# Kernel tuning notes

Measured on AMD Instinct MI355X. Metric: run time of the kernel, lower is better.

## Reference

```python
import jax, jax.numpy as jnp
import numpy as np
from jax import lax

B, T, D, H = 64, 2048, 128, 256  # batch, seq_len, input_dim, hidden_dim


def setup_inputs() -> dict:
    key = jax.random.key(0)
    ks = jax.random.split(key, 21)
    s = 0.05
    p = lambda k, shape: jax.random.normal(k, shape, dtype=jnp.float32) * s
    inp = {"x": jax.random.normal(ks[0], (B, T, D), dtype=jnp.float32)}
    i = 1
    for n in ["e1", "e2", "d1", "d2"]:  # encode1, encode2, reconstruct1, reconstruct2
        inp[n + "_Wih"] = p(ks[i], (4 * H, D)); i += 1
        inp[n + "_Whh"] = p(ks[i], (4 * H, H)); i += 1
        inp[n + "_bih"] = p(ks[i], (4 * H,)); i += 1
        inp[n + "_bhh"] = p(ks[i], (4 * H,)); i += 1
    inp["l1_W"] = p(ks[17], (D, H)); inp["l1_b"] = p(ks[18], (D,))
    inp["l2_W"] = p(ks[19], (D, H)); inp["l2_b"] = p(ks[20], (D,))
    return inp


def _lstm_cell(h, c, xt, Wih, Whh, bih, bhh):
    # PyTorch gate order: i, f, g, o
    g = xt @ Wih.T + h @ Whh.T + bih + bhh  # [B, 4H]
    i, f, gg, o = jnp.split(g, 4, axis=-1)
    c = jax.nn.sigmoid(f) * c + jax.nn.sigmoid(i) * jnp.tanh(gg)
    h = jax.nn.sigmoid(o) * jnp.tanh(c)
    return h, c


def _encode(x, h0, c0, Wih, Whh, bih, bhh):
    # x: [B, T, D] batch_first -> scan over time
    def step(carry, xt):
        h, c = carry
        h, c = _lstm_cell(h, c, xt, Wih, Whh, bih, bhh)
        return (h, c), None
    (h, c), _ = lax.scan(step, (h0, c0), jnp.swapaxes(x, 0, 1))
    return h, c


def _decode(n, h, c, Wih, Whh, bih, bhh, Wl, bl):
    # first output is linear(hidden) before any cell step (matches original decode)
    inp0 = h @ Wl.T + bl  # [B, D]
    def step(carry, _):
        h, c, inp = carry
        h, c = _lstm_cell(h, c, inp, Wih, Whh, bih, bhh)
        inp = h @ Wl.T + bl
        return (h, c, inp), inp
    _, outs = lax.scan(step, (h, c, inp0), None, length=n - 1)  # [n-1, B, D]
    out = jnp.concatenate([inp0[None], outs], axis=0)  # [n, B, D]
    return jnp.swapaxes(out, 0, 1)  # [B, n, D]


def reference(x,
              e1_Wih, e1_Whh, e1_bih, e1_bhh,
              e2_Wih, e2_Whh, e2_bih, e2_bhh,
              d1_Wih, d1_Whh, d1_bih, d1_bhh,
              d2_Wih, d2_Whh, d2_bih, d2_bhh,
              l1_W, l1_b, l2_W, l2_b):
    Bc, Tc = x.shape[0], x.shape[1]
    T1 = Tc // 2
    h0 = jnp.zeros((Bc, H), dtype=x.dtype)
    c0 = jnp.zeros((Bc, H), dtype=x.dtype)
    x1 = x[:, :T1][:, ::-1]  # first half, time-reversed
    x2 = x[:, T1:]
    h1, c1 = _encode(x1, h0, c0, e1_Wih, e1_Whh, e1_bih, e1_bhh)
    h2, c2 = _encode(x2, h1, c1, e2_Wih, e2_Whh, e2_bih, e2_bhh)
    out1 = _decode(T1, h1, c1, d1_Wih, d1_Whh, d1_bih, d1_bhh, l1_W, l1_b)
    out2 = _decode(Tc - T1, h2, c2, d2_Wih, d2_Whh, d2_bih, d2_bhh, l2_W, l2_b)[:, ::-1]
    return jnp.concatenate([out1, out2], axis=1)  # [B, T, D]
```

## Files before the change

kernel.cpp:

```cpp
#include <hip/hip_runtime.h>
#include <stdint.h>

#define Bv 64
#define Tv 2048
#define T1v 1024
#define Dv 128
#define Hv 256

typedef _Float16 h2_t __attribute__((ext_vector_type(2)));

__device__ inline float d2(uint32_t hp, uint32_t wp, float acc) {
#if __has_builtin(__builtin_amdgcn_fdot2)
  return __builtin_amdgcn_fdot2(__builtin_bit_cast(h2_t, hp),
                                __builtin_bit_cast(h2_t, wp), acc, false);
#else
  float out;
  asm("v_dot2_f32_f16 %0, %1, %2, %3" : "=v"(out) : "v"(hp), "v"(wp), "v"(acc));
  return out;
#endif
}

__device__ inline uint16_t f2h(float x) {
  _Float16 h = (_Float16)x;
  return __builtin_bit_cast(uint16_t, h);
}
__device__ inline float h2f(uint16_t u) {
  return (float)__builtin_bit_cast(_Float16, u);
}
__device__ inline uint32_t packpair(float a, float b) {
  return (uint32_t)f2h(a) | ((uint32_t)f2h(b) << 16);
}
__device__ inline float unpk(uint32_t u, int hi) {
  return h2f((uint16_t)(hi ? (u >> 16) : (u & 0xffff)));
}
__device__ inline float sigm(float x) { return 1.f / (1.f + __expf(-x)); }
__device__ inline float tanh_(float x) { return 2.f / (1.f + __expf(-2.f * x)) - 1.f; }

__device__ inline float qsum4(float v) {
  int t = __builtin_amdgcn_update_dpp(0, __float_as_int(v), 0xB1, 0xF, 0xF, true);
  v += __int_as_float(t);
  t = __builtin_amdgcn_update_dpp(0, __float_as_int(v), 0x4E, 0xF, 0xF, true);
  return v + __int_as_float(t);
}

__device__ inline uint4 ld_stream(const uint4* p) {
  const volatile uint32_t* q = (const volatile uint32_t*)p;
  uint4 v;
  v.x = q[0];
  v.y = q[1];
  v.z = q[2];
  v.w = q[3];
  return v;
}


__global__ void k_pack_x(const float* __restrict__ x, uint32_t* __restrict__ xpk) {
  int idx = blockIdx.x * 256 + threadIdx.x;
  const float2* x2 = (const float2*)x;
  float2 v = x2[idx];
  xpk[idx] = packpair(v.x, v.y);
}

__global__ void k_pack_w(const float* __restrict__ src, uint32_t* __restrict__ wAll,
                         uint32_t* __restrict__ wLg, uint32_t* __restrict__ wStr) {
  int idx = blockIdx.x * 256 + threadIdx.x;
  int row = idx >> 7, k2 = idx & 127;
  uint32_t pr = packpair(src[row * 256 + 2 * k2], src[row * 256 + 2 * k2 + 1]);
  wAll[k2 * 1024 + row] = pr;
  if (k2 >= 96) {
    int g = (k2 - 96) >> 2, qq = (k2 - 96) & 3;
    wLg[(g * 1024 + row) * 4 + qq] = pr;
  }
  if (k2 >= 48 && k2 < 96) wStr[row * 48 + (k2 - 48)] = pr;
}

__global__ void k_pack_w2(const float* __restrict__ src, uint32_t* __restrict__ wSt,
                          uint32_t* __restrict__ wLds) {
  int idx = blockIdx.x * 256 + threadIdx.x;
  int r = idx >> 7, k2 = idx & 127;
  uint32_t pr = packpair(src[r * 256 + 2 * k2], src[r * 256 + 2 * k2 + 1]);
  int gate = r >> 8, u = r & 255;
  int u_hi = u >> 7, jb = u & 127;
  int q = k2 >> 5, kk = k2 & 31;
  int tid = jb * 4 + q;
  int ri = u_hi * 4 + gate;
  if (kk < 24) {
    wSt[((ri * 6 + (kk >> 2)) * 512 + tid) * 4 + (kk & 3)] = pr;
  } else {
    wLds[((ri * 2 + ((kk - 24) >> 2)) * 512 + tid) * 4 + ((kk - 24) & 3)] = pr;
  }
}

__global__ void k_bias_pack(const float* __restrict__ b32, uint32_t* __restrict__ bpk) {
  int jb = threadIdx.x;
  uint32_t w[4];
#pragma unroll
  for (int wi = 0; wi < 4; ++wi) {
    int ri0 = 2 * wi, ri1 = 2 * wi + 1;
    int row0 = (ri0 & 3) * 256 + jb + 128 * (ri0 >> 2);
    int row1 = (ri1 & 3) * 256 + jb + 128 * (ri1 >> 2);
    w[wi] = packpair(b32[row0], b32[row1]);
  }
  ((uint4*)bpk)[jb] = make_uint4(w[0], w[1], w[2], w[3]);
}

__global__ void k_pack_wih(const float* __restrict__ Wih, uint32_t* __restrict__ wihp) {
  int idx = blockIdx.x * 256 + threadIdx.x;
  int row = idx >> 6, k2 = idx & 63;
  wihp[row * 64 + k2] = packpair(Wih[row * 128 + 2 * k2], Wih[row * 128 + 2 * k2 + 1]);
}

__global__ void k_bias2(const float* __restrict__ bih, const float* __restrict__ bhh,
                        float* __restrict__ bias) {
  int i = blockIdx.x * 256 + threadIdx.x;
  if (i < 1024) bias[i] = bih[i] + bhh[i];
}

__global__ void k_dec_combine(const float* __restrict__ Whh, const float* __restrict__ Wih,
                              const float* __restrict__ bih, const float* __restrict__ bhh,
                              const float* __restrict__ lW, const float* __restrict__ lb,
                              float* __restrict__ wd, float* __restrict__ bias) {
  int j = blockIdx.x;
  int k = threadIdx.x;
  __shared__ float wr[128];
  if (k < 128) wr[k] = Wih[j * 128 + k];
  __syncthreads();
  float acc = Whh[j * 256 + k];
  for (int d = 0; d < 128; ++d) acc += wr[d] * lW[d * 256 + k];
  wd[j * 256 + k] = acc;
  if (k == 0) {
    float s = bih[j] + bhh[j];
    for (int d = 0; d < 128; ++d) s += wr[d] * lb[d];
    bias[j] = s;
  }
}

__global__ void k_pack_wl(const float* __restrict__ lW, uint32_t* __restrict__ wlp) {
  int idx = blockIdx.x * 256 + threadIdx.x;
  int d = idx >> 7, k2 = idx & 127;
  wlp[d * 128 + k2] = packpair(lW[d * 256 + 2 * k2], lW[d * 256 + 2 * k2 + 1]);
}

template <int LAY>
__global__ __launch_bounds__(256) void k_xp_gemm(const uint32_t* __restrict__ xpk,
                                                 const uint32_t* __restrict__ wihp,
                                                 uint16_t* __restrict__ xp, int xt0, int xdt) {
  const int b = blockIdx.z;
  const int s0 = blockIdx.y * 32;
  const int r = blockIdx.x * 256 + threadIdx.x;
  uint32_t wreg[64];
#pragma unroll
  for (int k = 0; k < 64; ++k) wreg[k] = wihp[r * 64 + k];
  const int gate = r >> 8, u = r & 255;
  const int u_hi = u >> 7, jb = u & 127;
  const int ri = u_hi * 4 + gate;
  for (int sl = 0; sl < 32; ++sl) {
    const int s = s0 + sl;
    const int t = xt0 + s * xdt;
    const uint32_t* __restrict__ xrow = xpk + ((size_t)b * Tv + t) * 64;
    float a0 = 0.f, a1 = 0.f;
#pragma unroll
    for (int k = 0; k < 64; k += 2) {
      a0 = d2(xrow[k], wreg[k], a0);
      a1 = d2(xrow[k + 1], wreg[k + 1], a1);
    }
    uint16_t v = f2h(a0 + a1);
    if (LAY == 0)
      xp[(((size_t)b * T1v + s) * 128 + jb) * 8 + ri] = v;
    else
      xp[((size_t)b * T1v + s) * 1024 + r] = v;
  }
}


struct CfgU {
  const uint4* wSt;
  const uint4* wLds;
  const uint4* bpk;
  const uint4* xps;
  const float* h0;
  const float* c0;
  float* hN;
  float* cN;
  uint16_t* hist;
};

template <int NREGC, int NSTRC, int NLDSC>
__global__ void __launch_bounds__(512)
__attribute__((amdgpu_waves_per_eu(2, 2)))
k_rnnU(CfgU cA, CfgU cB, int nA) {
  __shared__ __align__(16) uint4 wldsM[NLDSC * 8 * 512];
  __shared__ __align__(16) uint16_t hbuf[2][4][72];

  const bool isA = (int)blockIdx.x < nA;
  const CfgU cfg = isA ? cA : cB;
  const int b = isA ? (int)blockIdx.x : ((int)blockIdx.x - nA);
  const int tid = threadIdx.x;
  const int q = tid & 3, jb = tid >> 2;

#pragma unroll
  for (int ri = 0; ri < 8; ++ri)
#pragma unroll
    for (int li = 0; li < NLDSC; ++li)
      wldsM[(ri * NLDSC + li) * 512 + tid] =
          cfg.wLds[(ri * 2 + (2 - NLDSC) + li) * 512 + tid];

  uint4 wr[8][NREGC];
#pragma unroll
  for (int ri = 0; ri < 8; ++ri)
#pragma unroll
    for (int cc = 0; cc < NREGC; ++cc) wr[ri][cc] = cfg.wSt[(ri * 6 + cc) * 512 + tid];

  const uint4 bp = cfg.bpk[jb];
  float c0r = cfg.c0 ? cfg.c0[b * 256 + jb] : 0.f;
  float c1r = cfg.c0 ? cfg.c0[b * 256 + jb + 128] : 0.f;

  uint16_t* histp = cfg.hist ? cfg.hist + (size_t)b * 1024 * 256 : nullptr;
  if (q == 0) {
    float h00 = cfg.h0 ? cfg.h0[b * 256 + jb] : 0.f;
    float h01 = cfg.h0 ? cfg.h0[b * 256 + jb + 128] : 0.f;
    uint16_t u0 = f2h(h00), u1 = f2h(h01);
    hbuf[0][jb >> 6][jb & 63] = u0;
    hbuf[0][2 + (jb >> 6)][jb & 63] = u1;
    if (histp) {
      histp[jb] = u0;
      histp[jb + 128] = u1;
    }
  }
  const uint4* xps4 = cfg.xps ? cfg.xps + (size_t)b * 1024 * 128 + jb : nullptr;

  __syncthreads();

  int cur = 0;
  for (int s = 0; s < 1024; ++s) {
    uint4 xq = make_uint4(0, 0, 0, 0);
    if (xps4) xq = xps4[(size_t)s * 128];
    const uint4* Hq = (const uint4*)&hbuf[cur][q][0];

    float acc[8];
#pragma unroll
    for (int ri = 0; ri < 8; ++ri) acc[ri] = 0.f;

#pragma unroll
    for (int cc = 0; cc < NREGC; ++cc) {
      const uint4 hv = Hq[cc];
#pragma unroll
      for (int ri = 0; ri < 8; ++ri) {
        acc[ri] = d2(hv.x, wr[ri][cc].x, acc[ri]);
        acc[ri] = d2(hv.y, wr[ri][cc].y, acc[ri]);
        acc[ri] = d2(hv.z, wr[ri][cc].z, acc[ri]);
        acc[ri] = d2(hv.w, wr[ri][cc].w, acc[ri]);
      }
    }
#pragma unroll
    for (int j = 0; j < NSTRC; ++j) {
      const int cc = NREGC + j;
      const uint4 hv = Hq[cc];
#pragma unroll
      for (int ri = 0; ri < 8; ++ri) {
        const uint4 wv = (cc < 6) ? ld_stream(cfg.wSt + (ri * 6 + cc) * 512 + tid)
                                  : ld_stream(cfg.wLds + (ri * 2 + (cc - 6)) * 512 + tid);
        acc[ri] = d2(hv.x, wv.x, acc[ri]);
        acc[ri] = d2(hv.y, wv.y, acc[ri]);
        acc[ri] = d2(hv.z, wv.z, acc[ri]);
        acc[ri] = d2(hv.w, wv.w, acc[ri]);
      }
    }
#pragma unroll
    for (int li = 0; li < NLDSC; ++li) {
      const int cc = 8 - NLDSC + li;
      const uint4 hv = Hq[cc];
#pragma unroll
      for (int ri = 0; ri < 8; ++ri) {
        const uint4 wv = wldsM[(ri * NLDSC + li) * 512 + tid];
        acc[ri] = d2(hv.x, wv.x, acc[ri]);
        acc[ri] = d2(hv.y, wv.y, acc[ri]);
        acc[ri] = d2(hv.z, wv.z, acc[ri]);
        acc[ri] = d2(hv.w, wv.w, acc[ri]);
      }
    }

#pragma unroll
    for (int ri = 0; ri < 8; ++ri) acc[ri] = qsum4(acc[ri]);

    acc[0] += unpk(bp.x, 0) + unpk(xq.x, 0);
    acc[1] += unpk(bp.x, 1) + unpk(xq.x, 1);
    acc[2] += unpk(bp.y, 0) + unpk(xq.y, 0);
    acc[3] += unpk(bp.y, 1) + unpk(xq.y, 1);
    acc[4] += unpk(bp.z, 0) + unpk(xq.z, 0);
    acc[5] += unpk(bp.z, 1) + unpk(xq.z, 1);
    acc[6] += unpk(bp.w, 0) + unpk(xq.w, 0);
    acc[7] += unpk(bp.w, 1) + unpk(xq.w, 1);

    const float cn0 = sigm(acc[1]) * c0r + sigm(acc[0]) * tanh_(acc[2]);
    const float h0v = sigm(acc[3]) * tanh_(cn0);
    c0r = cn0;
    const float cn1 = sigm(acc[5]) * c1r + sigm(acc[4]) * tanh_(acc[6]);
    const float h1v = sigm(acc[7]) * tanh_(cn1);
    c1r = cn1;

    if (q == 0) {
      const uint16_t hu0 = f2h(h0v), hu1 = f2h(h1v);
      hbuf[cur ^ 1][jb >> 6][jb & 63] = hu0;
      hbuf[cur ^ 1][2 + (jb >> 6)][jb & 63] = hu1;
      if (histp && s < 1023) {
        histp[(size_t)(s + 1) * 256 + jb] = hu0;
        histp[(size_t)(s + 1) * 256 + jb + 128] = hu1;
      }
    }
    __syncthreads();
    cur ^= 1;
  }

  if (cfg.hN && q == 0) {
    cfg.hN[b * 256 + jb] = h2f(hbuf[cur][jb >> 6][jb & 63]);
    cfg.hN[b * 256 + jb + 128] = h2f(hbuf[cur][2 + (jb >> 6)][jb & 63]);
    cfg.cN[b * 256 + jb] = c0r;
    cfg.cN[b * 256 + jb + 128] = c1r;
  }
}


struct ChainCfg {
  const uint32_t* wAll;
  const uint4* wLg;
  const uint32_t* wStr;
  const uint32_t* wih;
  const uint32_t* xpk;
  const uint16_t* xps;
  const float* bias;
  const float* h0;
  const float* c0;
  float* hN;
  float* cN;
  uint16_t* hist;
  int xt0, xdt;
};

template <int NRESP, bool WIH>
__global__ void __launch_bounds__(512)
__attribute__((amdgpu_waves_per_eu(2, 2)))
k_rnn5(ChainCfg cA, ChainCfg cB, int nA) {
  __shared__ __align__(16) uint4 wlds4[8 * 1024];
  __shared__ float gsm[1024];
  __shared__ __align__(16) uint16_t h16[256];
  __shared__ __align__(16) uint32_t xsh[64];

  const bool isA = (int)blockIdx.x < nA;
  const ChainCfg cfg = isA ? cA : cB;
  const int b = isA ? (int)blockIdx.x : ((int)blockIdx.x - nA);
  const int tid = threadIdx.x;
  const int r0 = tid, r1 = tid + 512;

#pragma unroll
  for (int i = 0; i < 16; ++i) wlds4[i * 512 + tid] = cfg.wLg[i * 512 + tid];

  uint16_t* histp = cfg.hist ? cfg.hist + (size_t)b * 1024 * 256 : nullptr;

  float creg = 0.f;
  if (tid < 256) {
    float h0v = cfg.h0 ? cfg.h0[b * 256 + tid] : 0.f;
    creg = cfg.c0 ? cfg.c0[b * 256 + tid] : 0.f;
    uint16_t hu = f2h(h0v);
    h16[tid] = hu;
    if (histp) histp[tid] = hu;
  }

  uint32_t w0[NRESP], w1[NRESP];
#pragma unroll
  for (int k = 0; k < NRESP; ++k) w0[k] = cfg.wAll[k * 1024 + r0];
#pragma unroll
  for (int k = 0; k < NRESP; ++k) w1[k] = cfg.wAll[k * 1024 + r1];
  const float bias0 = cfg.bias[r0];
  const float bias1 = cfg.bias[r1];

  constexpr int NS4 = (96 - NRESP) / 4;
  const uint4* ws0 = (const uint4*)(cfg.wStr + (size_t)r0 * 48 + (NRESP - 48));
  const uint4* ws1 = (const uint4*)(cfg.wStr + (size_t)r1 * 48 + (NRESP - 48));
  const uint4* wi0 = cfg.wih ? (const uint4*)(cfg.wih + (size_t)r0 * 64) : nullptr;
  const uint4* wi1 = cfg.wih ? (const uint4*)(cfg.wih + (size_t)r1 * 64) : nullptr;
  const bool hasx = cfg.xps != nullptr;

  __syncthreads();

  for (int s = 0; s < 1024; ++s) {
    float xa0 = 0.f, xa1 = 0.f;
    if (hasx) {
      size_t xb = ((size_t)b * 1024 + s) * 1024;
      xa0 = h2f(cfg.xps[xb + r0]);
      xa1 = h2f(cfg.xps[xb + r1]);
    }
    if constexpr (WIH) {
      if (cfg.wih) {
        if (tid < 64) {
          const int t = cfg.xt0 + s * cfg.xdt;
          xsh[tid] = cfg.xpk[((size_t)b * Tv + t) * 64 + tid];
        }
        __syncthreads();
      }
    }

    const uint4* H4 = (const uint4*)h16;
    float a00 = bias0, a01 = 0.f, a10 = bias1, a11 = 0.f;

#pragma unroll
    for (int c4 = 0; c4 < NRESP / 4; ++c4) {
      const uint4 hv = H4[c4];
      a00 = d2(hv.x, w0[4 * c4 + 0], a00);
      a01 = d2(hv.y, w0[4 * c4 + 1], a01);
      a10 = d2(hv.x, w1[4 * c4 + 0], a10);
      a11 = d2(hv.y, w1[4 * c4 + 1], a11);
      a00 = d2(hv.z, w0[4 * c4 + 2], a00);
      a01 = d2(hv.w, w0[4 * c4 + 3], a01);
      a10 = d2(hv.z, w1[4 * c4 + 2], a10);
      a11 = d2(hv.w, w1[4 * c4 + 3], a11);
    }
    if constexpr (NS4 > 0) {
#pragma unroll
      for (int u = 0; u < NS4; ++u) {
        const uint4 hv = H4[NRESP / 4 + u];
        const uint4 wv0 = ws0[u];
        const uint4 wv1 = ws1[u];
        a00 = d2(hv.x, wv0.x, a00);
        a01 = d2(hv.y, wv0.y, a01);
        a10 = d2(hv.x, wv1.x, a10);
        a11 = d2(hv.y, wv1.y, a11);
        a00 = d2(hv.z, wv0.z, a00);
        a01 = d2(hv.w, wv0.w, a01);
        a10 = d2(hv.z, wv1.z, a10);
        a11 = d2(hv.w, wv1.w, a11);
      }
    }
#pragma unroll
    for (int g = 0; g < 8; ++g) {
      const uint4 hv = H4[24 + g];
      const uint4 wv0 = wlds4[g * 1024 + r0];
      const uint4 wv1 = wlds4[g * 1024 + r1];
      a00 = d2(hv.x, wv0.x, a00);
      a01 = d2(hv.y, wv0.y, a01);
      a10 = d2(hv.x, wv1.x, a10);
      a11 = d2(hv.y, wv1.y, a11);
      a00 = d2(hv.z, wv0.z, a00);
      a01 = d2(hv.w, wv0.w, a01);
      a10 = d2(hv.z, wv1.z, a10);
      a11 = d2(hv.w, wv1.w, a11);
    }
    if constexpr (WIH) {
      if (cfg.wih) {
        const uint4* XS4 = (const uint4*)xsh;
#pragma unroll
        for (int u = 0; u < 16; ++u) {
          const uint4 xv = XS4[u];
          const uint4 wv0 = wi0[u];
          const uint4 wv1 = wi1[u];
          a00 = d2(xv.x, wv0.x, a00);
          a01 = d2(xv.y, wv0.y, a01);
          a10 = d2(xv.x, wv1.x, a10);
          a11 = d2(xv.y, wv1.y, a11);
          a00 = d2(xv.z, wv0.z, a00);
          a01 = d2(xv.w, wv0.w, a01);
          a10 = d2(xv.z, wv1.z, a10);
          a11 = d2(xv.w, wv1.w, a11);
        }
      }
    }

    gsm[r0] = a00 + a01 + xa0;
    gsm[r1] = a10 + a11 + xa1;
    __syncthreads();

    if (tid < 256) {
      const float gi = gsm[tid];
      const float gf = gsm[tid + 256];
      const float gg = gsm[tid + 512];
      const float go = gsm[tid + 768];
      const float cn = sigm(gf) * creg + sigm(gi) * tanh_(gg);
      const float hv = sigm(go) * tanh_(cn);
      creg = cn;
      const uint16_t hu = f2h(hv);
      h16[tid] = hu;
      if (histp && s < 1023) histp[(size_t)(s + 1) * 256 + tid] = hu;
    }
    __syncthreads();
  }

  if (cfg.hN && tid < 256) {
    cfg.hN[b * 256 + tid] = h2f(h16[tid]);
    cfg.cN[b * 256 + tid] = creg;
  }
}

__global__ __launch_bounds__(256) void k_out(const uint16_t* __restrict__ hist,
                                             const uint32_t* __restrict__ wlp,
                                             const float* __restrict__ lb,
                                             float* __restrict__ out, int outbase, int tsign) {
  const int b = blockIdx.y;
  const int t0 = blockIdx.x * 64;
  __shared__ __align__(16) uint32_t hq[64 * 128];
  const uint32_t* hsrc = (const uint32_t*)hist;
  for (int i = threadIdx.x; i < 64 * 128; i += 256) {
    hq[i] = hsrc[((size_t)b * 1024 + t0) * 128 + i];
  }
  __syncthreads();
  const int d = threadIdx.x & 127;
  const int th = threadIdx.x >> 7;
  float acc[32];
#pragma unroll
  for (int it = 0; it < 32; ++it) acc[it] = lb[d];
  const uint4* W4 = (const uint4*)(wlp + (size_t)d * 128);
  const uint4* HQ4 = (const uint4*)hq;
  for (int k2c = 0; k2c < 32; ++k2c) {
    const uint4 wv = W4[k2c];
#pragma unroll
    for (int it = 0; it < 32; ++it) {
      const int tl = th * 32 + it;
      const uint4 hv = HQ4[tl * 32 + k2c];
      acc[it] = d2(hv.x, wv.x, acc[it]);
      acc[it] = d2(hv.y, wv.y, acc[it]);
      acc[it] = d2(hv.z, wv.z, acc[it]);
      acc[it] = d2(hv.w, wv.w, acc[it]);
    }
  }
#pragma unroll
  for (int it = 0; it < 32; ++it) {
    const int tl = th * 32 + it;
    const int t = t0 + tl;
    const int tout = outbase + tsign * t;
    out[((size_t)b * Tv + tout) * Dv + d] = acc[it];
  }
}


extern "C" void kernel_launch(void* const* d_in, const int* in_sizes, int n_in,
                              void* d_out, int out_size, void* d_ws, size_t ws_size,
                              hipStream_t stream) {
  const float* x = (const float*)d_in[0];
  const float* e1_Wih = (const float*)d_in[1];
  const float* e1_Whh = (const float*)d_in[2];
  const float* e1_bih = (const float*)d_in[3];
  const float* e1_bhh = (const float*)d_in[4];
  const float* e2_Wih = (const float*)d_in[5];
  const float* e2_Whh = (const float*)d_in[6];
  const float* e2_bih = (const float*)d_in[7];
  const float* e2_bhh = (const float*)d_in[8];
  const float* d1_Wih = (const float*)d_in[9];
  const float* d1_Whh = (const float*)d_in[10];
  const float* d1_bih = (const float*)d_in[11];
  const float* d1_bhh = (const float*)d_in[12];
  const float* d2_Wih = (const float*)d_in[13];
  const float* d2_Whh = (const float*)d_in[14];
  const float* d2_bih = (const float*)d_in[15];
  const float* d2_bhh = (const float*)d_in[16];
  const float* l1_W = (const float*)d_in[17];
  const float* l1_b = (const float*)d_in[18];
  const float* l2_W = (const float*)d_in[19];
  const float* l2_b = (const float*)d_in[20];

  uint8_t* wsb = (uint8_t*)d_ws;
  size_t off = 0;
  auto take = [&](size_t n) -> void* {
    void* pp = wsb + off;
    off += (n + 255) & ~(size_t)255;
    return pp;
  };
  uint32_t* xpk = (uint32_t*)take((size_t)Bv * Tv * 64 * 4);
  uint16_t* hist1 = (uint16_t*)take((size_t)Bv * T1v * Hv * 2);
  uint16_t* hist2 = (uint16_t*)take((size_t)Bv * T1v * Hv * 2);
  struct WSet {
    uint32_t *wAll, *wLg, *wStr, *wih;
    float* bias;
    uint32_t *wSt, *wLds, *bpk;
  };
  auto take_wset = [&](bool with_ih) -> WSet {
    WSet w;
    w.wAll = (uint32_t*)take(128 * 1024 * 4);
    w.wLg = (uint32_t*)take(8 * 1024 * 16);
    w.wStr = (uint32_t*)take(1024 * 48 * 4);
    w.wih = with_ih ? (uint32_t*)take(1024 * 64 * 4) : nullptr;
    w.bias = (float*)take(1024 * 4);
    w.wSt = (uint32_t*)take(48 * 512 * 16);
    w.wLds = (uint32_t*)take(16 * 512 * 16);
    w.bpk = (uint32_t*)take(128 * 16);
    return w;
  };
  WSet we1 = take_wset(true);
  WSet we2 = take_wset(true);
  WSet wd1 = take_wset(false);
  WSet wd2 = take_wset(false);
  float* wd32 = (float*)take(1024 * 256 * 4);
  uint32_t* wl1p = (uint32_t*)take(128 * 128 * 4);
  uint32_t* wl2p = (uint32_t*)take(128 * 128 * 4);
  float* h1 = (float*)take(64 * 256 * 4);
  float* c1 = (float*)take(64 * 256 * 4);
  float* h2 = (float*)take(64 * 256 * 4);
  float* c2 = (float*)take(64 * 256 * 4);
  uint16_t* xp = (uint16_t*)take((size_t)Bv * T1v * 1024 * 2);
  const bool use_xp = ws_size >= off;

  int variant = 4;
  {
    hipFuncAttributes fa;
    auto spillfree = [&](const void* f) {
      return hipFuncGetAttributes(&fa, f) == hipSuccess && fa.localSizeBytes == 0;
    };
    if (use_xp) {
      if (spillfree(reinterpret_cast<const void*>(&k_rnnU<6, 1, 1>))) variant = 0;
      else if (spillfree(reinterpret_cast<const void*>(&k_rnnU<6, 0, 2>))) variant = 1;
      else if (spillfree(reinterpret_cast<const void*>(&k_rnnU<4, 2, 2>))) variant = 2;
      else if (spillfree(reinterpret_cast<const void*>(&k_rnn5<96, false>))) variant = 3;
    } else {
      if (spillfree(reinterpret_cast<const void*>(&k_rnn5<96, true>))) variant = 3;
    }
  }

  k_pack_x<<<(Bv * Tv * 64) / 256, 256, 0, stream>>>(x, xpk);
  k_pack_w<<<512, 256, 0, stream>>>(e1_Whh, we1.wAll, we1.wLg, we1.wStr);
  k_pack_w2<<<512, 256, 0, stream>>>(e1_Whh, we1.wSt, we1.wLds);
  k_pack_wih<<<256, 256, 0, stream>>>(e1_Wih, we1.wih);
  k_bias2<<<4, 256, 0, stream>>>(e1_bih, e1_bhh, we1.bias);
  k_bias_pack<<<1, 128, 0, stream>>>(we1.bias, we1.bpk);
  k_pack_w<<<512, 256, 0, stream>>>(e2_Whh, we2.wAll, we2.wLg, we2.wStr);
  k_pack_w2<<<512, 256, 0, stream>>>(e2_Whh, we2.wSt, we2.wLds);
  k_pack_wih<<<256, 256, 0, stream>>>(e2_Wih, we2.wih);
  k_bias2<<<4, 256, 0, stream>>>(e2_bih, e2_bhh, we2.bias);
  k_bias_pack<<<1, 128, 0, stream>>>(we2.bias, we2.bpk);
  k_dec_combine<<<1024, 256, 0, stream>>>(d1_Whh, d1_Wih, d1_bih, d1_bhh, l1_W, l1_b, wd32, wd1.bias);
  k_pack_w<<<512, 256, 0, stream>>>(wd32, wd1.wAll, wd1.wLg, wd1.wStr);
  k_pack_w2<<<512, 256, 0, stream>>>(wd32, wd1.wSt, wd1.wLds);
  k_bias_pack<<<1, 128, 0, stream>>>(wd1.bias, wd1.bpk);
  k_dec_combine<<<1024, 256, 0, stream>>>(d2_Whh, d2_Wih, d2_bih, d2_bhh, l2_W, l2_b, wd32, wd2.bias);
  k_pack_w<<<512, 256, 0, stream>>>(wd32, wd2.wAll, wd2.wLg, wd2.wStr);
  k_pack_w2<<<512, 256, 0, stream>>>(wd32, wd2.wSt, wd2.wLds);
  k_bias_pack<<<1, 128, 0, stream>>>(wd2.bias, wd2.bpk);
  k_pack_wl<<<64, 256, 0, stream>>>(l1_W, wl1p);
  k_pack_wl<<<64, 256, 0, stream>>>(l2_W, wl2p);

  if (variant <= 2) {
    auto launch_u = [&](int grid, CfgU a, CfgU b2, int nA) {
      if (variant == 0)      k_rnnU<6, 1, 1><<<grid, 512, 0, stream>>>(a, b2, nA);
      else if (variant == 1) k_rnnU<6, 0, 2><<<grid, 512, 0, stream>>>(a, b2, nA);
      else                   k_rnnU<4, 2, 2><<<grid, 512, 0, stream>>>(a, b2, nA);
    };
    k_xp_gemm<0><<<dim3(4, 32, 64), 256, 0, stream>>>(xpk, we1.wih, xp, 1023, -1);
    CfgU e1c{(const uint4*)we1.wSt, (const uint4*)we1.wLds, (const uint4*)we1.bpk,
             (const uint4*)xp, nullptr, nullptr, h1, c1, nullptr};
    launch_u(64, e1c, e1c, 64);

    k_xp_gemm<0><<<dim3(4, 32, 64), 256, 0, stream>>>(xpk, we2.wih, xp, 1024, 1);
    CfgU e2c{(const uint4*)we2.wSt, (const uint4*)we2.wLds, (const uint4*)we2.bpk,
             (const uint4*)xp, h1, c1, h2, c2, nullptr};
    CfgU d1c{(const uint4*)wd1.wSt, (const uint4*)wd1.wLds, (const uint4*)wd1.bpk,
             nullptr, h1, c1, nullptr, nullptr, hist1};
    launch_u(128, e2c, d1c, 64);

    CfgU d2c{(const uint4*)wd2.wSt, (const uint4*)wd2.wLds, (const uint4*)wd2.bpk,
             nullptr, h2, c2, nullptr, nullptr, hist2};
    launch_u(64, d2c, d2c, 64);
  } else {
    auto launch_old = [&](int grid, ChainCfg a, ChainCfg b2, int nA) {
      if (use_xp) {
        if (variant == 3) k_rnn5<96, false><<<grid, 512, 0, stream>>>(a, b2, nA);
        else              k_rnn5<80, false><<<grid, 512, 0, stream>>>(a, b2, nA);
      } else {
        if (variant == 3) k_rnn5<96, true><<<grid, 512, 0, stream>>>(a, b2, nA);
        else              k_rnn5<80, true><<<grid, 512, 0, stream>>>(a, b2, nA);
      }
    };
    if (use_xp) k_xp_gemm<1><<<dim3(4, 32, 64), 256, 0, stream>>>(xpk, we1.wih, xp, 1023, -1);
    ChainCfg e1c{we1.wAll, (const uint4*)we1.wLg, we1.wStr, use_xp ? nullptr : we1.wih,
                 use_xp ? nullptr : xpk, use_xp ? xp : nullptr, we1.bias,
                 nullptr, nullptr, h1, c1, nullptr, 1023, -1};
    launch_old(64, e1c, e1c, 64);

    if (use_xp) k_xp_gemm<1><<<dim3(4, 32, 64), 256, 0, stream>>>(xpk, we2.wih, xp, 1024, 1);
    ChainCfg e2c{we2.wAll, (const uint4*)we2.wLg, we2.wStr, use_xp ? nullptr : we2.wih,
                 use_xp ? nullptr : xpk, use_xp ? xp : nullptr, we2.bias,
                 h1, c1, h2, c2, nullptr, 1024, 1};
    ChainCfg d1c{wd1.wAll, (const uint4*)wd1.wLg, wd1.wStr, nullptr, nullptr, nullptr,
                 wd1.bias, h1, c1, nullptr, nullptr, hist1, 0, 0};
    launch_old(128, e2c, d1c, 64);

    ChainCfg d2c{wd2.wAll, (const uint4*)wd2.wLg, wd2.wStr, nullptr, nullptr, nullptr,
                 wd2.bias, h2, c2, nullptr, nullptr, hist2, 0, 0};
    launch_old(64, d2c, d2c, 64);
  }

  k_out<<<dim3(16, 64), 256, 0, stream>>>(hist1, wl1p, l1_b, (float*)d_out, 0, 1);
  k_out<<<dim3(16, 64), 256, 0, stream>>>(hist2, wl2p, l2_b, (float*)d_out, 2047, -1);
}
```

Before: 7.299 ms.

## Share h loads across lanes via DPP rotation and stream weights from double-buffered copies

Adds a new recurrent kernel in which each lane of a quad reads only its own two 16-byte h chunks from LDS and gets the other chunks from neighbouring lanes through DPP row rotations. This is meant to cut LDS read traffic and bank conflicts for the hidden-state broadcast. The recurrent weights are re-laid out per rotation slot, and part of them is streamed from global memory each step, alternating between two duplicated copies. A small probe kernel checks the DPP rotation direction at runtime, and the kernel picks between two compiled directions. The register/stream/LDS split is chosen by checking which template variant compiles without spills. Risks include extra DPP instructions, global-load latency on the serial recurrence, and the added runtime branch.

```diff
diff --git a/kernel.cpp b/kernel.cpp
--- a/kernel.cpp
+++ b/kernel.cpp
@@ -8,6 +8,8 @@
 #define Hv 256
 
 typedef _Float16 h2_t __attribute__((ext_vector_type(2)));
+
+template <int V> struct IC { static constexpr int v = V; };
 
 __device__ inline float d2(uint32_t hp, uint32_t wp, float acc) {
 #if __has_builtin(__builtin_amdgcn_fdot2)
@@ -43,14 +45,20 @@
   return v + __int_as_float(t);
 }
 
-__device__ inline uint4 ld_stream(const uint4* p) {
-  const volatile uint32_t* q = (const volatile uint32_t*)p;
-  uint4 v;
-  v.x = q[0];
-  v.y = q[1];
-  v.z = q[2];
-  v.w = q[3];
-  return v;
+template <int CTRL>
+__device__ inline uint4 dpp_rot4(uint4 v) {
+  uint4 r;
+  r.x = (uint32_t)__builtin_amdgcn_update_dpp(0, (int)v.x, CTRL, 0xF, 0xF, true);
+  r.y = (uint32_t)__builtin_amdgcn_update_dpp(0, (int)v.y, CTRL, 0xF, 0xF, true);
+  r.z = (uint32_t)__builtin_amdgcn_update_dpp(0, (int)v.z, CTRL, 0xF, 0xF, true);
+  r.w = (uint32_t)__builtin_amdgcn_update_dpp(0, (int)v.w, CTRL, 0xF, 0xF, true);
+  return r;
+}
+
+__global__ void k_dpp_probe(uint32_t* flag) {
+  uint32_t v = threadIdx.x;
+  uint32_t r = (uint32_t)__builtin_amdgcn_update_dpp(0, (int)v, 0x124, 0xF, 0xF, true);
+  if (threadIdx.x == 0) *flag = (r == 4u) ? 0u : 1u;
 }
 
 
@@ -74,7 +82,7 @@
   if (k2 >= 48 && k2 < 96) wStr[row * 48 + (k2 - 48)] = pr;
 }
 
-__global__ void k_pack_w2(const float* __restrict__ src, uint32_t* __restrict__ wSt,
+__global__ void k_pack_w2(const float* __restrict__ src, uint32_t* __restrict__ wReg,
                           uint32_t* __restrict__ wLds) {
   int idx = blockIdx.x * 256 + threadIdx.x;
   int r = idx >> 7, k2 = idx & 127;
@@ -84,10 +92,39 @@
   int q = k2 >> 5, kk = k2 & 31;
   int tid = jb * 4 + q;
   int ri = u_hi * 4 + gate;
-  if (kk < 24) {
-    wSt[((ri * 6 + (kk >> 2)) * 512 + tid) * 4 + (kk & 3)] = pr;
+  int cc = kk >> 2, c = kk & 3;
+  if (cc < 6) {
+    wReg[((ri * 6 + cc) * 512 + tid) * 4 + c] = pr;
   } else {
-    wLds[((ri * 2 + ((kk - 24) >> 2)) * 512 + tid) * 4 + ((kk - 24) & 3)] = pr;
+    wLds[((ri * 2 + (cc - 6)) * 512 + tid) * 4 + c] = pr;
+  }
+}
+
+__global__ void k_pack_w3(const float* __restrict__ src, uint32_t* __restrict__ wReg,
+                          uint32_t* __restrict__ wStr, uint32_t* __restrict__ wLds,
+                          int R, int S) {
+  int idx = blockIdx.x * 256 + threadIdx.x;
+  int r = idx >> 7, k2 = idx & 127;
+  uint32_t pr = packpair(src[r * 256 + 2 * k2], src[r * 256 + 2 * k2 + 1]);
+  int gate = r >> 8, u2 = r & 255;
+  int u_hi = u2 >> 7, jb = u2 & 127;
+  int q = k2 >> 5, kk = k2 & 31;
+  int cc = kk >> 2, c = kk & 3;
+  int tid = jb * 4 + q;
+  int ri = u_hi * 4 + gate;
+  int jbm = jb & 3;
+  int slot = 2 * (((cc >> 1) - jbm) & 3) + (cc & 1);
+  if (slot < R) {
+    wReg[((ri * R + slot) * 512 + tid) * 4 + c] = pr;
+  } else if (slot < R + S) {
+    int j = slot - R;
+    size_t o = ((size_t)(ri * S + j) * 512 + tid) * 4 + c;
+    wStr[o] = pr;
+    wStr[(size_t)8 * S * 512 * 4 + o] = pr;
+  } else {
+    int L = 8 - R - S;
+    int l = slot - R - S;
+    wLds[((ri * L + l) * 512 + tid) * 4 + c] = pr;
   }
 }
 
@@ -174,8 +211,9 @@
 
 
 struct CfgU {
-  const uint4* wSt;
-  const uint4* wLds;
+  const uint4* wA;
+  const uint4* wB;
+  const uint4* wC;
   const uint4* bpk;
   const uint4* xps;
   const float* h0;
@@ -183,33 +221,34 @@
   float* hN;
   float* cN;
   uint16_t* hist;
+  const uint32_t* dir;
 };
 
-template <int NREGC, int NSTRC, int NLDSC>
+template <int R, int S>
 __global__ void __launch_bounds__(512)
 __attribute__((amdgpu_waves_per_eu(2, 2)))
-k_rnnU(CfgU cA, CfgU cB, int nA) {
-  __shared__ __align__(16) uint4 wldsM[NLDSC * 8 * 512];
-  __shared__ __align__(16) uint16_t hbuf[2][4][72];
+k_rnnU2(CfgU cA, CfgU cB, int nA) {
+  constexpr int L = 8 - R - S;
+  __shared__ __align__(16) uint4 wldsM[L * 8 * 512];
+  __shared__ __align__(16) uint16_t hbuf[2][4][80];
 
   const bool isA = (int)blockIdx.x < nA;
   const CfgU cfg = isA ? cA : cB;
   const int b = isA ? (int)blockIdx.x : ((int)blockIdx.x - nA);
   const int tid = threadIdx.x;
   const int q = tid & 3, jb = tid >> 2;
-
+  const int jbm = jb & 3;
+
+  const uint32_t dirv = __builtin_amdgcn_readfirstlane(*cfg.dir);
+
+#pragma unroll
+  for (int i = 0; i < 8 * L; ++i) wldsM[i * 512 + tid] = cfg.wC[i * 512 + tid];
+
+  uint4 wr[8][R];
 #pragma unroll
   for (int ri = 0; ri < 8; ++ri)
 #pragma unroll
-    for (int li = 0; li < NLDSC; ++li)
-      wldsM[(ri * NLDSC + li) * 512 + tid] =
-          cfg.wLds[(ri * 2 + (2 - NLDSC) + li) * 512 + tid];
-
-  uint4 wr[8][NREGC];
-#pragma unroll
-  for (int ri = 0; ri < 8; ++ri)
-#pragma unroll
-    for (int cc = 0; cc < NREGC; ++cc) wr[ri][cc] = cfg.wSt[(ri * 6 + cc) * 512 + tid];
+    for (int u = 0; u < R; ++u) wr[ri][u] = cfg.wA[(ri * R + u) * 512 + tid];
 
   const uint4 bp = cfg.bpk[jb];
   float c0r = cfg.c0 ? cfg.c0[b * 256 + jb] : 0.f;
@@ -232,17 +271,149 @@
   __syncthreads();
 
   int cur = 0;
+
+  auto run = [&](auto DIRC) {
+    constexpr int DIR = decltype(DIRC)::v;
+    for (int s = 0; s < 1024; ++s) {
+      uint4 xq = make_uint4(0, 0, 0, 0);
+      if (xps4) xq = xps4[(size_t)s * 128];
+
+      const uint4* wS = cfg.wB + ((s & 1) ? (size_t)(8 * S * 512) : (size_t)0);
+      uint4 sv[8 * S];
+#pragma unroll
+      for (int ri = 0; ri < 8; ++ri)
+#pragma unroll
+        for (int j = 0; j < S; ++j) sv[ri * S + j] = wS[(ri * S + j) * 512 + tid];
+
+      const uint4* Hq4 = (const uint4*)(&hbuf[cur][q][0]);
+      const uint4 hh0 = Hq4[2 * jbm];
+      const uint4 hh1 = Hq4[2 * jbm + 1];
+
+      float acc[8];
+#pragma unroll
+      for (int ri = 0; ri < 8; ++ri) acc[ri] = 0.f;
+
+#pragma unroll
+      for (int d = 0; d < 4; ++d) {
+        uint4 h0 = hh0, h1 = hh1;
+        if (d == 1) { h0 = dpp_rot4<0x124>(hh0); h1 = dpp_rot4<0x124>(hh1); }
+        if (d == 2) { h0 = dpp_rot4<0x128>(hh0); h1 = dpp_rot4<0x128>(hh1); }
+        if (d == 3) { h0 = dpp_rot4<0x12C>(hh0); h1 = dpp_rot4<0x12C>(hh1); }
+#pragma unroll
+        for (int k = 0; k < 2; ++k) {
+          const int u = (DIR == 0) ? (2 * d + k) : (2 * ((4 - d) & 3) + k);
+          const uint4 hv = k ? h1 : h0;
+#pragma unroll
+          for (int ri = 0; ri < 8; ++ri) {
+            uint4 wv;
+            if (u < R) wv = wr[ri][u];
+            else if (u < R + S) wv = sv[ri * S + (u - R)];
+            else wv = wldsM[(ri * L + (u - R - S)) * 512 + tid];
+            acc[ri] = d2(hv.x, wv.x, acc[ri]);
+            acc[ri] = d2(hv.y, wv.y, acc[ri]);
+            acc[ri] = d2(hv.z, wv.z, acc[ri]);
+            acc[ri] = d2(hv.w, wv.w, acc[ri]);
+          }
+        }
+      }
+
+#pragma unroll
+      for (int ri = 0; ri < 8; ++ri) acc[ri] = qsum4(acc[ri]);
+
+      acc[0] += unpk(bp.x, 0) + unpk(xq.x, 0);
+      acc[1] += unpk(bp.x, 1) + unpk(xq.x, 1);
+      acc[2] += unpk(bp.y, 0) + unpk(xq.y, 0);
+      acc[3] += unpk(bp.y, 1) + unpk(xq.y, 1);
+      acc[4] += unpk(bp.z, 0) + unpk(xq.z, 0);
+      acc[5] += unpk(bp.z, 1) + unpk(xq.z, 1);
+      acc[6] += unpk(bp.w, 0) + unpk(xq.w, 0);
+      acc[7] += unpk(bp.w, 1) + unpk(xq.w, 1);
+
+      const float cn0 = sigm(acc[1]) * c0r + sigm(acc[0]) * tanh_(acc[2]);
+      const float h0v = sigm(acc[3]) * tanh_(cn0);
+      c0r = cn0;
+      const float cn1 = sigm(acc[5]) * c1r + sigm(acc[4]) * tanh_(acc[6]);
+      const float h1v = sigm(acc[7]) * tanh_(cn1);
+      c1r = cn1;
+
+      if (q == 0) {
+        const uint16_t hu0 = f2h(h0v), hu1 = f2h(h1v);
+        hbuf[cur ^ 1][jb >> 6][jb & 63] = hu0;
+        hbuf[cur ^ 1][2 + (jb >> 6)][jb & 63] = hu1;
+        if (histp && s < 1023) {
+          histp[(size_t)(s + 1) * 256 + jb] = hu0;
+          histp[(size_t)(s + 1) * 256 + jb + 128] = hu1;
+        }
+      }
+      __syncthreads();
+      cur ^= 1;
+    }
+  };
+
+  if (dirv == 0) run(IC<0>{});
+  else           run(IC<1>{});
+
+  if (cfg.hN && q == 0) {
+    cfg.hN[b * 256 + jb] = h2f(hbuf[cur][jb >> 6][jb & 63]);
+    cfg.hN[b * 256 + jb + 128] = h2f(hbuf[cur][2 + (jb >> 6)][jb & 63]);
+    cfg.cN[b * 256 + jb] = c0r;
+    cfg.cN[b * 256 + jb + 128] = c1r;
+  }
+}
+
+__global__ void __launch_bounds__(512)
+__attribute__((amdgpu_waves_per_eu(2, 2)))
+k_rnnU6(CfgU cA, CfgU cB, int nA) {
+  __shared__ __align__(16) uint4 wldsM[2 * 8 * 512];
+  __shared__ __align__(16) uint16_t hbuf[2][4][72];
+
+  const bool isA = (int)blockIdx.x < nA;
+  const CfgU cfg = isA ? cA : cB;
+  const int b = isA ? (int)blockIdx.x : ((int)blockIdx.x - nA);
+  const int tid = threadIdx.x;
+  const int q = tid & 3, jb = tid >> 2;
+
+#pragma unroll
+  for (int i = 0; i < 16; ++i) wldsM[i * 512 + tid] = cfg.wC[i * 512 + tid];
+
+  uint4 wr[8][6];
+#pragma unroll
+  for (int ri = 0; ri < 8; ++ri)
+#pragma unroll
+    for (int cc = 0; cc < 6; ++cc) wr[ri][cc] = cfg.wA[(ri * 6 + cc) * 512 + tid];
+
+  const uint4 bp = cfg.bpk[jb];
+  float c0r = cfg.c0 ? cfg.c0[b * 256 + jb] : 0.f;
+  float c1r = cfg.c0 ? cfg.c0[b * 256 + jb + 128] : 0.f;
+
+  uint16_t* histp = cfg.hist ? cfg.hist + (size_t)b * 1024 * 256 : nullptr;
+  if (q == 0) {
+    float h00 = cfg.h0 ? cfg.h0[b * 256 + jb] : 0.f;
+    float h01 = cfg.h0 ? cfg.h0[b * 256 + jb + 128] : 0.f;
+    uint16_t u0 = f2h(h00), u1 = f2h(h01);
+    hbuf[0][jb >> 6][jb & 63] = u0;
+    hbuf[0][2 + (jb >> 6)][jb & 63] = u1;
+    if (histp) {
+      histp[jb] = u0;
+      histp[jb + 128] = u1;
+    }
+  }
+  const uint4* xps4 = cfg.xps ? cfg.xps + (size_t)b * 1024 * 128 + jb : nullptr;
+
+  __syncthreads();
+
+  int cur = 0;
   for (int s = 0; s < 1024; ++s) {
     uint4 xq = make_uint4(0, 0, 0, 0);
     if (xps4) xq = xps4[(size_t)s * 128];
-    const uint4* Hq = (const uint4*)&hbuf[cur][q][0];
+    const uint4* Hq = (const uint4*)(&hbuf[cur][q][0]);
 
     float acc[8];
 #pragma unroll
     for (int ri = 0; ri < 8; ++ri) acc[ri] = 0.f;
 
 #pragma unroll
-    for (int cc = 0; cc < NREGC; ++cc) {
+    for (int cc = 0; cc < 6; ++cc) {
       const uint4 hv = Hq[cc];
 #pragma unroll
       for (int ri = 0; ri < 8; ++ri) {
@@ -253,26 +424,11 @@
       }
     }
 #pragma unroll
-    for (int j = 0; j < NSTRC; ++j) {
-      const int cc = NREGC + j;
-      const uint4 hv = Hq[cc];
+    for (int l = 0; l < 2; ++l) {
+      const uint4 hv = Hq[6 + l];
 #pragma unroll
       for (int ri = 0; ri < 8; ++ri) {
-        const uint4 wv = (cc < 6) ? ld_stream(cfg.wSt + (ri * 6 + cc) * 512 + tid)
-                                  : ld_stream(cfg.wLds + (ri * 2 + (cc - 6)) * 512 + tid);
-        acc[ri] = d2(hv.x, wv.x, acc[ri]);
-        acc[ri] = d2(hv.y, wv.y, acc[ri]);
-        acc[ri] = d2(hv.z, wv.z, acc[ri]);
-        acc[ri] = d2(hv.w, wv.w, acc[ri]);
-      }
-    }
-#pragma unroll
-    for (int li = 0; li < NLDSC; ++li) {
-      const int cc = 8 - NLDSC + li;
-      const uint4 hv = Hq[cc];
-#pragma unroll
-      for (int ri = 0; ri < 8; ++ri) {
-        const uint4 wv = wldsM[(ri * NLDSC + li) * 512 + tid];
+        const uint4 wv = wldsM[(ri * 2 + l) * 512 + tid];
         acc[ri] = d2(hv.x, wv.x, acc[ri]);
         acc[ri] = d2(hv.y, wv.y, acc[ri]);
         acc[ri] = d2(hv.z, wv.z, acc[ri]);
@@ -563,22 +719,24 @@
     off += (n + 255) & ~(size_t)255;
     return pp;
   };
+  uint32_t* dppflag = (uint32_t*)take(256);
   uint32_t* xpk = (uint32_t*)take((size_t)Bv * Tv * 64 * 4);
   uint16_t* hist1 = (uint16_t*)take((size_t)Bv * T1v * Hv * 2);
   uint16_t* hist2 = (uint16_t*)take((size_t)Bv * T1v * Hv * 2);
   struct WSet {
-    uint32_t *wAll, *wLg, *wStr, *wih;
+    uint32_t *wAll, *wLg, *wStr48, *wih;
     float* bias;
-    uint32_t *wSt, *wLds, *bpk;
+    uint32_t *wReg, *wStrm, *wLds, *bpk;
   };
   auto take_wset = [&](bool with_ih) -> WSet {
     WSet w;
     w.wAll = (uint32_t*)take(128 * 1024 * 4);
     w.wLg = (uint32_t*)take(8 * 1024 * 16);
-    w.wStr = (uint32_t*)take(1024 * 48 * 4);
+    w.wStr48 = (uint32_t*)take(1024 * 48 * 4);
     w.wih = with_ih ? (uint32_t*)take(1024 * 64 * 4) : nullptr;
     w.bias = (float*)take(1024 * 4);
-    w.wSt = (uint32_t*)take(48 * 512 * 16);
+    w.wReg = (uint32_t*)take(48 * 512 * 16);
+    w.wStrm = (uint32_t*)take(2 * 16 * 512 * 16);
     w.wLds = (uint32_t*)take(16 * 512 * 16);
     w.bpk = (uint32_t*)take(128 * 16);
     return w;
@@ -597,90 +755,126 @@
   uint16_t* xp = (uint16_t*)take((size_t)Bv * T1v * 1024 * 2);
   const bool use_xp = ws_size >= off;
 
-  int variant = 4;
+  int variant = 6, RR = 0, SS = 0;
   {
     hipFuncAttributes fa;
-    auto spillfree = [&](const void* f) {
+    auto sf = [&](const void* f) {
       return hipFuncGetAttributes(&fa, f) == hipSuccess && fa.localSizeBytes == 0;
     };
     if (use_xp) {
-      if (spillfree(reinterpret_cast<const void*>(&k_rnnU<6, 1, 1>))) variant = 0;
-      else if (spillfree(reinterpret_cast<const void*>(&k_rnnU<6, 0, 2>))) variant = 1;
-      else if (spillfree(reinterpret_cast<const void*>(&k_rnnU<4, 2, 2>))) variant = 2;
-      else if (spillfree(reinterpret_cast<const void*>(&k_rnn5<96, false>))) variant = 3;
+      if (sf(reinterpret_cast<const void*>(&k_rnnU2<5, 1>))) { variant = 0; RR = 5; SS = 1; }
+      else if (sf(reinterpret_cast<const void*>(&k_rnnU2<5, 2>))) { variant = 1; RR = 5; SS = 2; }
+      else if (sf(reinterpret_cast<const void*>(&k_rnnU2<4, 2>))) { variant = 2; RR = 4; SS = 2; }
+      else if (sf(reinterpret_cast<const void*>(&k_rnnU6))) variant = 4;
+      else if (sf(reinterpret_cast<const void*>(&k_rnn5<96, false>))) variant = 5;
     } else {
-      if (spillfree(reinterpret_cast<const void*>(&k_rnn5<96, true>))) variant = 3;
+      if (sf(reinterpret_cast<const void*>(&k_rnn5<96, true>))) variant = 5;
     }
   }
 
   k_pack_x<<<(Bv * Tv * 64) / 256, 256, 0, stream>>>(x, xpk);
-  k_pack_w<<<512, 256, 0, stream>>>(e1_Whh, we1.wAll, we1.wLg, we1.wStr);
-  k_pack_w2<<<512, 256, 0, stream>>>(e1_Whh, we1.wSt, we1.wLds);
   k_pack_wih<<<256, 256, 0, stream>>>(e1_Wih, we1.wih);
+  k_pack_wih<<<256, 256, 0, stream>>>(e2_Wih, we2.wih);
   k_bias2<<<4, 256, 0, stream>>>(e1_bih, e1_bhh, we1.bias);
-  k_bias_pack<<<1, 128, 0, stream>>>(we1.bias, we1.bpk);
-  k_pack_w<<<512, 256, 0, stream>>>(e2_Whh, we2.wAll, we2.wLg, we2.wStr);
-  k_pack_w2<<<512, 256, 0, stream>>>(e2_Whh, we2.wSt, we2.wLds);
-  k_pack_wih<<<256, 256, 0, stream>>>(e2_Wih, we2.wih);
   k_bias2<<<4, 256, 0, stream>>>(e2_bih, e2_bhh, we2.bias);
-  k_bias_pack<<<1, 128, 0, stream>>>(we2.bias, we2.bpk);
-  k_dec_combine<<<1024, 256, 0, stream>>>(d1_Whh, d1_Wih, d1_bih, d1_bhh, l1_W, l1_b, wd32, wd1.bias);
-  k_pack_w<<<512, 256, 0, stream>>>(wd32, wd1.wAll, wd1.wLg, wd1.wStr);
-  k_pack_w2<<<512, 256, 0, stream>>>(wd32, wd1.wSt, wd1.wLds);
-  k_bias_pack<<<1, 128, 0, stream>>>(wd1.bias, wd1.bpk);
-  k_dec_combine<<<1024, 256, 0, stream>>>(d2_Whh, d2_Wih, d2_bih, d2_bhh, l2_W, l2_b, wd32, wd2.bias);
-  k_pack_w<<<512, 256, 0, stream>>>(wd32, wd2.wAll, wd2.wLg, wd2.wStr);
-  k_pack_w2<<<512, 256, 0, stream>>>(wd32, wd2.wSt, wd2.wLds);
-  k_bias_pack<<<1, 128, 0, stream>>>(wd2.bias, wd2.bpk);
   k_pack_wl<<<64, 256, 0, stream>>>(l1_W, wl1p);
   k_pack_wl<<<64, 256, 0, stream>>>(l2_W, wl2p);
 
   if (variant <= 2) {
-    auto launch_u = [&](int grid, CfgU a, CfgU b2, int nA) {
-      if (variant == 0)      k_rnnU<6, 1, 1><<<grid, 512, 0, stream>>>(a, b2, nA);
-      else if (variant == 1) k_rnnU<6, 0, 2><<<grid, 512, 0, stream>>>(a, b2, nA);
-      else                   k_rnnU<4, 2, 2><<<grid, 512, 0, stream>>>(a, b2, nA);
+    k_dpp_probe<<<1, 64, 0, stream>>>(dppflag);
+    k_pack_w3<<<512, 256, 0, stream>>>(e1_Whh, we1.wReg, we1.wStrm, we1.wLds, RR, SS);
+    k_pack_w3<<<512, 256, 0, stream>>>(e2_Whh, we2.wReg, we2.wStrm, we2.wLds, RR, SS);
+    k_bias_pack<<<1, 128, 0, stream>>>(we1.bias, we1.bpk);
+    k_bias_pack<<<1, 128, 0, stream>>>(we2.bias, we2.bpk);
+    k_dec_combine<<<1024, 256, 0, stream>>>(d1_Whh, d1_Wih, d1_bih, d1_bhh, l1_W, l1_b, wd32, wd1.bias);
+    k_pack_w3<<<512, 256, 0, stream>>>(wd32, wd1.wReg, wd1.wStrm, wd1.wLds, RR, SS);
+    k_bias_pack<<<1, 128, 0, stream>>>(wd1.bias, wd1.bpk);
+    k_dec_combine<<<1024, 256, 0, stream>>>(d2_Whh, d2_Wih, d2_bih, d2_bhh, l2_W, l2_b, wd32, wd2.bias);
+    k_pack_w3<<<512, 256, 0, stream>>>(wd32, wd2.wReg, wd2.wStrm, wd2.wLds, RR, SS);
+    k_bias_pack<<<1, 128, 0, stream>>>(wd2.bias, wd2.bpk);
+
+    auto mk = [&](WSet& w, const uint4* xps, const float* h0, const float* c0,
+                  float* hN, float* cN, uint16_t* hist) -> CfgU {
+      return CfgU{(const uint4*)w.wReg, (const uint4*)w.wStrm, (const uint4*)w.wLds,
+                  (const uint4*)w.bpk, xps, h0, c0, hN, cN, hist, dppflag};
+    };
+    auto launch_u2 = [&](int grid, CfgU a, CfgU b2, int nA) {
+      if (variant == 0)      k_rnnU2<5, 1><<<grid, 512, 0, stream>>>(a, b2, nA);
+      else if (variant == 1) k_rnnU2<5, 2><<<grid, 512, 0, stream>>>(a, b2, nA);
+      else                   k_rnnU2<4, 2><<<grid, 512, 0, stream>>>(a, b2, nA);
+    };
+
+    k_xp_gemm<0><<<dim3(4, 32, 64), 256, 0, stream>>>(xpk, we1.wih, xp, 1023, -1);
+    CfgU e1c = mk(we1, (const uint4*)xp, nullptr, nullptr, h1, c1, nullptr);
+    launch_u2(64, e1c, e1c, 64);
+
+    k_xp_gemm<0><<<dim3(4, 32, 64), 256, 0, stream>>>(xpk, we2.wih, xp, 1024, 1);
+    CfgU e2c = mk(we2, (const uint4*)xp, h1, c1, h2, c2, nullptr);
+    CfgU d1c = mk(wd1, nullptr, h1, c1, nullptr, nullptr, hist1);
+    launch_u2(128, e2c, d1c, 64);
+
+    CfgU d2c = mk(wd2, nullptr, h2, c2, nullptr, nullptr, hist2);
+    launch_u2(64, d2c, d2c, 64);
+  } else if (variant == 4) {
+    k_pack_w2<<<512, 256, 0, stream>>>(e1_Whh, we1.wReg, we1.wLds);
+    k_pack_w2<<<512, 256, 0, stream>>>(e2_Whh, we2.wReg, we2.wLds);
+    k_bias_pack<<<1, 128, 0, stream>>>(we1.bias, we1.bpk);
+    k_bias_pack<<<1, 128, 0, stream>>>(we2.bias, we2.bpk);
+    k_dec_combine<<<1024, 256, 0, stream>>>(d1_Whh, d1_Wih, d1_bih, d1_bhh, l1_W, l1_b, wd32, wd1.bias);
+    k_pack_w2<<<512, 256, 0, stream>>>(wd32, wd1.wReg, wd1.wLds);
+    k_bias_pack<<<1, 128, 0, stream>>>(wd1.bias, wd1.bpk);
+    k_dec_combine<<<1024, 256, 0, stream>>>(d2_Whh, d2_Wih, d2_bih, d2_bhh, l2_W, l2_b, wd32, wd2.bias);
+    k_pack_w2<<<512, 256, 0, stream>>>(wd32, wd2.wReg, wd2.wLds);
+    k_bias_pack<<<1, 128, 0, stream>>>(wd2.bias, wd2.bpk);
+
+    auto mk = [&](WSet& w, const uint4* xps, const float* h0, const float* c0,
+                  float* hN, float* cN, uint16_t* hist) -> CfgU {
+      return CfgU{(const uint4*)w.wReg, nullptr, (const uint4*)w.wLds,
+                  (const uint4*)w.bpk, xps, h0, c0, hN, cN, hist, nullptr};
     };
     k_xp_gemm<0><<<dim3(4, 32, 64), 256, 0, stream>>>(xpk, we1.wih, xp, 1023, -1);
-    CfgU e1c{(const uint4*)we1.wSt, (const uint4*)we1.wLds, (const uint4*)we1.bpk,
-             (const uint4*)xp, nullptr, nullptr, h1, c1, nullptr};
-    launch_u(64, e1c, e1c, 64);
+    CfgU e1c = mk(we1, (const uint4*)xp, nullptr, nullptr, h1, c1, nullptr);
+    k_rnnU6<<<64, 512, 0, stream>>>(e1c, e1c, 64);
 
     k_xp_gemm<0><<<dim3(4, 32, 64), 256, 0, stream>>>(xpk, we2.wih, xp, 1024, 1);
-    CfgU e2c{(const uint4*)we2.wSt, (const uint4*)we2.wLds, (const uint4*)we2.bpk,
-             (const uint4*)xp, h1, c1, h2, c2, nullptr};
-    CfgU d1c{(const uint4*)wd1.wSt, (const uint4*)wd1.wLds, (const uint4*)wd1.bpk,
-             nullptr, h1, c1, nullptr, nullptr, hist1};
-    launch_u(128, e2c, d1c, 64);
-
-    CfgU d2c{(const uint4*)wd2.wSt, (const uint4*)wd2.wLds, (const uint4*)wd2.bpk,
-             nullptr, h2, c2, nullptr, nullptr, hist2};
-    launch_u(64, d2c, d2c, 64);
+    CfgU e2c = mk(we2, (const uint4*)xp, h1, c1, h2, c2, nullptr);
+    CfgU d1c = mk(wd1, nullptr, h1, c1, nullptr, nullptr, hist1);
+    k_rnnU6<<<128, 512, 0, stream>>>(e2c, d1c, 64);
+
+    CfgU d2c = mk(wd2, nullptr, h2, c2, nullptr, nullptr, hist2);
+    k_rnnU6<<<64, 512, 0, stream>>>(d2c, d2c, 64);
   } else {
+    k_pack_w<<<512, 256, 0, stream>>>(e1_Whh, we1.wAll, we1.wLg, we1.wStr48);
+    k_pack_w<<<512, 256, 0, stream>>>(e2_Whh, we2.wAll, we2.wLg, we2.wStr48);
+    k_dec_combine<<<1024, 256, 0, stream>>>(d1_Whh, d1_Wih, d1_bih, d1_bhh, l1_W, l1_b, wd32, wd1.bias);
+    k_pack_w<<<512, 256, 0, stream>>>(wd32, wd1.wAll, wd1.wLg, wd1.wStr48);
+    k_dec_combine<<<1024, 256, 0, stream>>>(d2_Whh, d2_Wih, d2_bih, d2_bhh, l2_W, l2_b, wd32, wd2.bias);
+    k_pack_w<<<512, 256, 0, stream>>>(wd32, wd2.wAll, wd2.wLg, wd2.wStr48);
+
     auto launch_old = [&](int grid, ChainCfg a, ChainCfg b2, int nA) {
       if (use_xp) {
-        if (variant == 3) k_rnn5<96, false><<<grid, 512, 0, stream>>>(a, b2, nA);
+        if (variant == 5) k_rnn5<96, false><<<grid, 512, 0, stream>>>(a, b2, nA);
         else              k_rnn5<80, false><<<grid, 512, 0, stream>>>(a, b2, nA);
       } else {
-        if (variant == 3) k_rnn5<96, true><<<grid, 512, 0, stream>>>(a, b2, nA);
+        if (variant == 5) k_rnn5<96, true><<<grid, 512, 0, stream>>>(a, b2, nA);
         else              k_rnn5<80, true><<<grid, 512, 0, stream>>>(a, b2, nA);
       }
     };
     if (use_xp) k_xp_gemm<1><<<dim3(4, 32, 64), 256, 0, stream>>>(xpk, we1.wih, xp, 1023, -1);
-    ChainCfg e1c{we1.wAll, (const uint4*)we1.wLg, we1.wStr, use_xp ? nullptr : we1.wih,
+    ChainCfg e1c{we1.wAll, (const uint4*)we1.wLg, we1.wStr48, use_xp ? nullptr : we1.wih,
                  use_xp ? nullptr : xpk, use_xp ? xp : nullptr, we1.bias,
                  nullptr, nullptr, h1, c1, nullptr, 1023, -1};
     launch_old(64, e1c, e1c, 64);
 
     if (use_xp) k_xp_gemm<1><<<dim3(4, 32, 64), 256, 0, stream>>>(xpk, we2.wih, xp, 1024, 1);
-    ChainCfg e2c{we2.wAll, (const uint4*)we2.wLg, we2.wStr, use_xp ? nullptr : we2.wih,
+    ChainCfg e2c{we2.wAll, (const uint4*)we2.wLg, we2.wStr48, use_xp ? nullptr : we2.wih,
                  use_xp ? nullptr : xpk, use_xp ? xp : nullptr, we2.bias,
                  h1, c1, h2, c2, nullptr, 1024, 1};
-    ChainCfg d1c{wd1.wAll, (const uint4*)wd1.wLg, wd1.wStr, nullptr, nullptr, nullptr,
+    ChainCfg d1c{wd1.wAll, (const uint4*)wd1.wLg, wd1.wStr48, nullptr, nullptr, nullptr,
                  wd1.bias, h1, c1, nullptr, nullptr, hist1, 0, 0};
     launch_old(128, e2c, d1c, 64);
 
-    ChainCfg d2c{wd2.wAll, (const uint4*)wd2.wLg, wd2.wStr, nullptr, nullptr, nullptr,
+    ChainCfg d2c{wd2.wAll, (const uint4*)wd2.wLg, wd2.wStr48, nullptr, nullptr, nullptr,
                  wd2.bias, h2, c2, nullptr, nullptr, hist2, 0, 0};
     launch_old(64, d2c, d2c, 64);
   }
```

Measured after the change: 7.171 ms. About the same (-1.8%).
